# Optimization experiments

Measured on AMD Instinct MI355X. Metric: run time of the kernel, lower is better.

## Reference

```python
import jax, jax.numpy as jnp
import numpy as np

N_NODES = 50000
N_REL = 8
D_IN = 128
D_OUT = 128
N_EDGES = 800000


def setup_inputs() -> dict:
    key = jax.random.key(0)
    k = jax.random.split(key, 6)
    # Xavier-ish scales for the learned params
    w_scale = (6.0 / (D_IN + D_OUT)) ** 0.5
    X = jax.random.normal(k[0], (N_NODES, D_IN), dtype=jnp.float32)
    W = jax.random.uniform(k[1], (N_REL, D_IN, D_OUT), dtype=jnp.float32,
                           minval=-w_scale, maxval=w_scale)
    W0 = jax.random.uniform(k[2], (D_IN, D_OUT), dtype=jnp.float32,
                            minval=-w_scale, maxval=w_scale)
    inv_norm = jnp.ones((N_REL, N_NODES), dtype=jnp.float32)  # init'd to ones in torch
    # COO edge list encoding the stacked sparse adjacency tensor adj_tensor[r, dst, src]
    edge_src = jax.random.randint(k[3], (N_EDGES,), 0, N_NODES, dtype=jnp.int32)
    edge_dst = jax.random.randint(k[4], (N_EDGES,), 0, N_NODES, dtype=jnp.int32)
    edge_rel = jax.random.randint(k[5], (N_EDGES,), 0, N_REL, dtype=jnp.int32)
    return {"X": X, "W": W, "W0": W0, "inv_norm": inv_norm,
            "edge_src": edge_src, "edge_dst": edge_dst, "edge_rel": edge_rel}


def reference(X, W, W0, inv_norm, edge_src, edge_dst, edge_rel) -> jnp.ndarray:
    # Per relation r:  inv_norm[r][:,None] * (A_r @ (X @ W[r]))  ; summed over r
    R, N = inv_norm.shape
    # Dense per-relation transform: [R, N, D_OUT]
    XW = jnp.einsum('nd,rde->rne', X, W)
    # Sparse A_r @ XW_r as gather over source nodes + scatter-add into (rel, dst)
    msgs = XW[edge_rel, edge_src]                       # [E, D_OUT]
    seg_ids = edge_rel * N + edge_dst                   # combined (rel, dst) segment id
    agg = jax.ops.segment_sum(msgs, seg_ids, num_segments=R * N)
    agg = agg.reshape(R, N, -1)                         # [R, N, D_OUT]
    incoming = jnp.sum(agg * inv_norm[:, :, None], axis=0)  # [N, D_OUT]
    self_connection = X @ W0
    return incoming + self_connection
```

## Files before the change

kernel.cpp:

```cpp
#include <hip/hip_runtime.h>

typedef __attribute__((ext_vector_type(8))) short short8;
typedef __attribute__((ext_vector_type(4))) float f32x4;

__device__ __forceinline__ unsigned short f2bf(float f) {
    unsigned u = __float_as_uint(f);
    u += 0x7FFF + ((u >> 16) & 1);
    return (unsigned short)(u >> 16);
}

__device__ __forceinline__ float readlane_f(float v, int l) {
    return __int_as_float(__builtin_amdgcn_readlane(__float_as_int(v), l));
}

__device__ __forceinline__ float bflo(unsigned u) { return __uint_as_float(u << 16); }
__device__ __forceinline__ float bfhi(unsigned u) { return __uint_as_float(u & 0xFFFF0000u); }

#define CHB 2048
__global__ __launch_bounds__(256) void chist_kernel(
    const int* __restrict__ edst, int* __restrict__ ccounts, int E, int C)
{
    __shared__ int lh[CHB];
    const int t = threadIdx.x;
    for (int i = t; i < C; i += 256) lh[i] = 0;
    __syncthreads();
    const int base = blockIdx.x * 2048;
    const int end = min(base + 2048, E);
    for (int i = base + t; i < end; i += 256)
        atomicAdd(&lh[edst[i] >> 8], 1);
    __syncthreads();
    for (int i = t; i < C; i += 256)
        if (lh[i]) atomicAdd(&ccounts[i], lh[i]);
}

__global__ __launch_bounds__(256) void cscan_kernel(
    const int* __restrict__ ccounts, int* __restrict__ cstarts,
    int* __restrict__ cursor, int C)
{
    __shared__ int sd[256];
    const int t = threadIdx.x;
    const int per = (C + 255) >> 8;
    int c[8]; int s = 0;
#pragma unroll
    for (int k = 0; k < 8; ++k) {
        const int idx = t * per + k;
        c[k] = (k < per && idx < C) ? ccounts[idx] : 0;
        s += c[k];
    }
    sd[t] = s; __syncthreads();
    for (int off = 1; off < 256; off <<= 1) {
        int x = (t >= off) ? sd[t - off] : 0;
        __syncthreads();
        sd[t] += x;
        __syncthreads();
    }
    int run = sd[t] - s;
#pragma unroll
    for (int k = 0; k < 8; ++k) {
        const int idx = t * per + k;
        if (k < per && idx < C) { cstarts[idx] = run; cursor[idx] = run; }
        run += c[k];
    }
}

#define PART_EPB 2048
__global__ __launch_bounds__(256) void partition_kernel(
    const int* __restrict__ esrc, const int* __restrict__ edst,
    const int* __restrict__ erel, int* __restrict__ cursor,
    unsigned* __restrict__ staged, int E, int C)
{
    __shared__ int lh[CHB];
    const int t = threadIdx.x;
    const int base = blockIdx.x * PART_EPB;
    const int end = min(base + PART_EPB, E);

    for (int i = t; i < C; i += 256) lh[i] = 0;
    __syncthreads();
    for (int i = base + t; i < end; i += 256)
        atomicAdd(&lh[edst[i] >> 8], 1);
    __syncthreads();
    for (int i = t; i < C; i += 256) {
        const int c = lh[i];
        lh[i] = c ? atomicAdd(&cursor[i], c) : 0;
    }
    __syncthreads();
    for (int i = base + t; i < end; i += 256) {
        const int d = edst[i];
        const int pos = atomicAdd(&lh[d >> 8], 1);
        staged[pos] = (unsigned)esrc[i] | ((unsigned)(d & 255) << 21)
                    | ((unsigned)erel[i] << 29);
    }
}

__global__ __launch_bounds__(256) void binsort_kernel(
    const unsigned* __restrict__ staged, const int* __restrict__ cstarts,
    int* __restrict__ starts, unsigned* __restrict__ sorted,
    int N, int E, int C)
{
    __shared__ int lcur[2048];
    __shared__ int wsum[256];
    const int b = blockIdx.x;
    const int t = threadIdx.x;
    const int d0 = b << 8;
    const int binBase = d0 * 8;
    const int nbins = (min(d0 + 256, N) - d0) * 8;
    const int base = cstarts[b];
    const int end = (b + 1 < C) ? cstarts[b + 1] : E;

    for (int i = t; i < 2048; i += 256) lcur[i] = 0;
    __syncthreads();
    for (int i = base + t; i < end; i += 256) {
        const unsigned v = staged[i];
        atomicAdd(&lcur[(int)((v >> 21) & 255u) * 8 + (int)(v >> 29)], 1);
    }
    __syncthreads();
    const int b8 = t * 8;
    int c[8]; int s = 0;
#pragma unroll
    for (int k = 0; k < 8; ++k) { c[k] = lcur[b8 + k]; s += c[k]; }
    wsum[t] = s; __syncthreads();
    for (int off = 1; off < 256; off <<= 1) {
        int x = (t >= off) ? wsum[t - off] : 0;
        __syncthreads();
        wsum[t] += x;
        __syncthreads();
    }
    int run = wsum[t] - s + base;
#pragma unroll
    for (int k = 0; k < 8; ++k) {
        lcur[b8 + k] = run;
        if (b8 + k < nbins) starts[binBase + b8 + k] = run;
        run += c[k];
    }
    __syncthreads();
    for (int i = base + t; i < end; i += 256) {
        const unsigned v = staged[i];
        const unsigned src = v & 0x1FFFFFu;
        const unsigned rel = v >> 29;
        const int pos = atomicAdd(&lcur[(int)((v >> 21) & 255u) * 8 + (int)rel], 1);
        sorted[pos] = src | (rel << 28);
    }
}

__global__ __launch_bounds__(256) void cast_kernel(
    const float* __restrict__ X, const float* __restrict__ W,
    const float* __restrict__ W0, unsigned short* __restrict__ Xb,
    unsigned short* __restrict__ Bt, int M, int R)
{
    const int ktot = (R + 1) * 128;
    const int nx = M * 32;
    const int idx = blockIdx.x * 256 + threadIdx.x;
    if (idx < nx) {
        const float4 v = ((const float4*)X)[idx];
        uint2 p;
        p.x = (unsigned)f2bf(v.x) | ((unsigned)f2bf(v.y) << 16);
        p.y = (unsigned)f2bf(v.z) | ((unsigned)f2bf(v.w) << 16);
        *(uint2*)(Xb + (size_t)idx * 4) = p;
    } else if (idx < nx + 128 * ktot) {
        const int e = idx - nx;
        const int n = e / ktot;
        const int k = e - n * ktot;
        const float v = (k < R * 128) ? W[(size_t)k * 128 + n]
                                      : W0[(size_t)(k - R * 128) * 128 + n];
        Bt[(size_t)n * ktot + k] = f2bf(v);
    }
}

#define ACC(P, U) switch ((P) >> 28) {                                   \
        case 0: ax0 += bflo(U); ay0 += bfhi(U); break;                   \
        case 1: ax1 += bflo(U); ay1 += bfhi(U); break;                   \
        case 2: ax2 += bflo(U); ay2 += bfhi(U); break;                   \
        case 3: ax3 += bflo(U); ay3 += bfhi(U); break;                   \
        case 4: ax4 += bflo(U); ay4 += bfhi(U); break;                   \
        case 5: ax5 += bflo(U); ay5 += bfhi(U); break;                   \
        case 6: ax6 += bflo(U); ay6 += bfhi(U); break;                   \
        default: ax7 += bflo(U); ay7 += bfhi(U); break; }

__global__ __launch_bounds__(256) void aggregate_kernel(
    const unsigned short* __restrict__ Xb, const float* __restrict__ inv_norm,
    const unsigned* __restrict__ sorted, const int* __restrict__ starts,
    unsigned short* __restrict__ A, int N, int E)
{
    const int dst = (int)((blockIdx.x * blockDim.x + threadIdx.x) >> 6);
    if (dst >= N) return;
    const int lane = threadIdx.x & 63;

    const int start = starts[dst * 8];
    const int end = (dst + 1 < N) ? starts[dst * 8 + 8] : E;

    float ax0=0,ay0=0, ax1=0,ay1=0, ax2=0,ay2=0, ax3=0,ay3=0;
    float ax4=0,ay4=0, ax5=0,ay5=0, ax6=0,ay6=0, ax7=0,ay7=0;

    for (int cb = start; cb < end; cb += 64) {
        const int take = min(64, end - cb);
        unsigned batch = 0;
        if (cb + lane < end) batch = sorted[cb + lane];
        int j = 0;
        for (; j + 8 <= take; j += 8) {
            unsigned p[8], u[8];
#pragma unroll
            for (int q = 0; q < 8; ++q)
                p[q] = (unsigned)__builtin_amdgcn_readlane((int)batch, j + q);
#pragma unroll
            for (int q = 0; q < 8; ++q)
                u[q] = ((const unsigned*)(Xb + ((size_t)(p[q] & 0x0FFFFFFFu) << 7)))[lane];
            ACC(p[0], u[0]); ACC(p[1], u[1]); ACC(p[2], u[2]); ACC(p[3], u[3]);
            ACC(p[4], u[4]); ACC(p[5], u[5]); ACC(p[6], u[6]); ACC(p[7], u[7]);
        }
        for (; j + 4 <= take; j += 4) {
            const unsigned p0 = (unsigned)__builtin_amdgcn_readlane((int)batch, j);
            const unsigned p1 = (unsigned)__builtin_amdgcn_readlane((int)batch, j + 1);
            const unsigned p2 = (unsigned)__builtin_amdgcn_readlane((int)batch, j + 2);
            const unsigned p3 = (unsigned)__builtin_amdgcn_readlane((int)batch, j + 3);
            const unsigned u0 = ((const unsigned*)(Xb + ((size_t)(p0 & 0x0FFFFFFFu) << 7)))[lane];
            const unsigned u1 = ((const unsigned*)(Xb + ((size_t)(p1 & 0x0FFFFFFFu) << 7)))[lane];
            const unsigned u2 = ((const unsigned*)(Xb + ((size_t)(p2 & 0x0FFFFFFFu) << 7)))[lane];
            const unsigned u3 = ((const unsigned*)(Xb + ((size_t)(p3 & 0x0FFFFFFFu) << 7)))[lane];
            ACC(p0, u0); ACC(p1, u1); ACC(p2, u2); ACC(p3, u3);
        }
        for (; j < take; ++j) {
            const unsigned p = (unsigned)__builtin_amdgcn_readlane((int)batch, j);
            const unsigned u = ((const unsigned*)(Xb + ((size_t)(p & 0x0FFFFFFFu) << 7)))[lane];
            ACC(p, u);
        }
    }

    const float nv_l = (lane < 8) ? inv_norm[(size_t)lane * N + dst] : 0.f;

    unsigned short* Arow = A + (size_t)dst * 1024 + lane * 2;
    {
        float s;
        s = readlane_f(nv_l, 0); *(unsigned*)(Arow + 0*128) = (unsigned)f2bf(ax0*s) | ((unsigned)f2bf(ay0*s) << 16);
        s = readlane_f(nv_l, 1); *(unsigned*)(Arow + 1*128) = (unsigned)f2bf(ax1*s) | ((unsigned)f2bf(ay1*s) << 16);
        s = readlane_f(nv_l, 2); *(unsigned*)(Arow + 2*128) = (unsigned)f2bf(ax2*s) | ((unsigned)f2bf(ay2*s) << 16);
        s = readlane_f(nv_l, 3); *(unsigned*)(Arow + 3*128) = (unsigned)f2bf(ax3*s) | ((unsigned)f2bf(ay3*s) << 16);
        s = readlane_f(nv_l, 4); *(unsigned*)(Arow + 4*128) = (unsigned)f2bf(ax4*s) | ((unsigned)f2bf(ay4*s) << 16);
        s = readlane_f(nv_l, 5); *(unsigned*)(Arow + 5*128) = (unsigned)f2bf(ax5*s) | ((unsigned)f2bf(ay5*s) << 16);
        s = readlane_f(nv_l, 6); *(unsigned*)(Arow + 6*128) = (unsigned)f2bf(ax6*s) | ((unsigned)f2bf(ay6*s) << 16);
        s = readlane_f(nv_l, 7); *(unsigned*)(Arow + 7*128) = (unsigned)f2bf(ax7*s) | ((unsigned)f2bf(ay7*s) << 16);
    }
}

template <int KT>
__global__ __launch_bounds__(512) void gemm_kernel(
    const unsigned short* __restrict__ A, const unsigned short* __restrict__ Xb,
    const unsigned short* __restrict__ Bt, float* __restrict__ out, int M)
{
    constexpr int NI = KT / 64;
    constexpr int NA = (KT - 128) / 64;
    __shared__ unsigned short Asw[2][128 * 64];
    __shared__ unsigned short Bsw[2][128 * 64];

    const int tid = threadIdx.x;
    const int wave = tid >> 6;
    const int lane = tid & 63;
    const int ln = lane & 15, quad = lane >> 4;
    const int wm = wave & 3;
    const int wn = wave >> 2;
    const int m0 = blockIdx.x * 128;

    const int sr = tid >> 2;
    const int sq = tid & 3;
    int am = m0 + sr; if (am >= M) am = M - 1;
    const unsigned short* Ag = A  + (size_t)am * (KT - 128) + sq * 16;
    const unsigned short* Xg = Xb + (size_t)am * 128 + sq * 16;
    const unsigned short* Bg = Bt + (size_t)sr * KT + sq * 16;

    const int wofs0 = sr * 64 + ((((sq << 1) + 0) ^ (sr & 7)) << 3);
    const int wofs1 = sr * 64 + ((((sq << 1) + 1) ^ (sr & 7)) << 3);

    f32x4 acc[8] = {};
    short8 ra0, ra1, rb0, rb1;

    auto load_regs = [&](int ko) {
        const unsigned short* as = (ko < NA) ? (Ag + ko * 64) : (Xg + (ko - NA) * 64);
        ra0 = *(const short8*)(as);
        ra1 = *(const short8*)(as + 8);
        const unsigned short* bs = Bg + ko * 64;
        rb0 = *(const short8*)(bs);
        rb1 = *(const short8*)(bs + 8);
    };
    auto write_lds = [&](int buf) {
        *(short8*)&Asw[buf][wofs0] = ra0;
        *(short8*)&Asw[buf][wofs1] = ra1;
        *(short8*)&Bsw[buf][wofs0] = rb0;
        *(short8*)&Bsw[buf][wofs1] = rb1;
    };

    load_regs(0);
    write_lds(0);
    __syncthreads();

    int cur = 0;
#pragma unroll
    for (int ko = 0; ko < NI; ++ko) {
        if (ko + 1 < NI) load_regs(ko + 1);
        __builtin_amdgcn_sched_barrier(0);
#pragma unroll
        for (int ks = 0; ks < 2; ++ks) {
            short8 af[2], bf[4];
#pragma unroll
            for (int mi = 0; mi < 2; ++mi) {
                const int r = wm * 32 + mi * 16 + ln;
                af[mi] = *(const short8*)&Asw[cur][r * 64 + ((((ks << 2) + quad) ^ (r & 7)) << 3)];
            }
#pragma unroll
            for (int ci = 0; ci < 4; ++ci) {
                const int r = wn * 64 + ci * 16 + ln;
                bf[ci] = *(const short8*)&Bsw[cur][r * 64 + ((((ks << 2) + quad) ^ (r & 7)) << 3)];
            }
#pragma unroll
            for (int mi = 0; mi < 2; ++mi)
#pragma unroll
                for (int ci = 0; ci < 4; ++ci)
                    acc[mi * 4 + ci] = __builtin_amdgcn_mfma_f32_16x16x32_bf16(
                        af[mi], bf[ci], acc[mi * 4 + ci], 0, 0, 0);
        }
        __builtin_amdgcn_sched_barrier(0);
        if (ko + 1 < NI) write_lds(cur ^ 1);
        __syncthreads();
        cur ^= 1;
    }

#pragma unroll
    for (int mi = 0; mi < 2; ++mi)
#pragma unroll
        for (int ci = 0; ci < 4; ++ci)
#pragma unroll
            for (int rg = 0; rg < 4; ++rg) {
                const int row = m0 + wm * 32 + mi * 16 + quad * 4 + rg;
                if (row < M)
                    out[(size_t)row * 128 + wn * 64 + ci * 16 + ln] = acc[mi * 4 + ci][rg];
            }
}

__global__ __launch_bounds__(256) void gemm_kernel_rt(
    const unsigned short* __restrict__ A, const unsigned short* __restrict__ Xb,
    const unsigned short* __restrict__ Bt, float* __restrict__ out,
    int M, int ktot)
{
    const int tid = threadIdx.x;
    const int wave = tid >> 6;
    const int lane = tid & 63;
    const int ln = lane & 15, quad = lane >> 4;
    const int m0 = blockIdx.x * 64 + wave * 16;
    int m = m0 + ln; if (m >= M) m = M - 1;
    const unsigned short* Arow = A + (size_t)m * (ktot - 128) + quad * 8;
    const unsigned short* Xrow = Xb + (size_t)m * 128 + quad * 8;
    const unsigned short* Bbase = Bt + (size_t)ln * ktot + quad * 8;

    f32x4 acc[8] = {};
    for (int kb = 0; kb < (ktot >> 5); ++kb) {
        const int k0 = kb << 5;
        const unsigned short* asrc = (k0 < ktot - 128) ? (Arow + k0) : (Xrow + (k0 - (ktot - 128)));
        const short8 a = *(const short8*)asrc;
#pragma unroll
        for (int c = 0; c < 8; ++c) {
            const short8 b = *(const short8*)(Bbase + (size_t)c * 16 * ktot + k0);
            acc[c] = __builtin_amdgcn_mfma_f32_16x16x32_bf16(a, b, acc[c], 0, 0, 0);
        }
    }
#pragma unroll
    for (int c = 0; c < 8; ++c) {
#pragma unroll
        for (int rg = 0; rg < 4; ++rg) {
            const int row = m0 + quad * 4 + rg;
            if (row < M) out[(size_t)row * 128 + c * 16 + ln] = acc[c][rg];
        }
    }
}

extern "C" void kernel_launch(void* const* d_in, const int* in_sizes, int n_in,
                              void* d_out, int out_size, void* d_ws, size_t ws_size,
                              hipStream_t stream) {
    const float* X        = (const float*)d_in[0];
    const float* W        = (const float*)d_in[1];
    const float* W0       = (const float*)d_in[2];
    const float* inv_norm = (const float*)d_in[3];
    const int*   esrc     = (const int*)d_in[4];
    const int*   edst     = (const int*)d_in[5];
    const int*   erel     = (const int*)d_in[6];
    float* out = (float*)d_out;

    const int N  = in_sizes[0] / 128;
    const int E  = in_sizes[4];
    const int R  = in_sizes[3] / N;
    const int KB = N * 8;
    const int ktot = (R + 1) * 128;
    const int C  = (N + 255) >> 8;

    char* ws = (char*)d_ws;
    size_t off = 0;
    auto alloc = [&](size_t bytes) -> char* {
        char* p = ws + off; off = (off + bytes + 255) & ~(size_t)255; return p;
    };
    unsigned short* A         = (unsigned short*)alloc((size_t)N * R * 128 * 2);
    unsigned short* Xb        = (unsigned short*)alloc((size_t)N * 128 * 2);
    unsigned short* Bt        = (unsigned short*)alloc((size_t)128 * ktot * 2);
    int*            ccounts   = (int*)alloc((size_t)C * 4);
    int*            cstarts   = (int*)alloc((size_t)C * 4);
    int*            cursor    = (int*)alloc((size_t)C * 4);
    int*            starts    = (int*)alloc((size_t)KB * 4);
    unsigned*       staged    = (unsigned*)alloc((size_t)E * 4);
    unsigned*       sorted    = (unsigned*)alloc((size_t)E * 4);
    (void)ws_size;

    const int nEdgeBlocks = (E + 2047) / 2048;

    hipMemsetAsync(ccounts, 0, (size_t)C * 4, stream);
    chist_kernel<<<nEdgeBlocks, 256, 0, stream>>>(edst, ccounts, E, C);
    cscan_kernel<<<1, 256, 0, stream>>>(ccounts, cstarts, cursor, C);
    partition_kernel<<<nEdgeBlocks, 256, 0, stream>>>(esrc, edst, erel, cursor, staged, E, C);
    binsort_kernel<<<C, 256, 0, stream>>>(staged, cstarts, starts, sorted, N, E, C);
    cast_kernel<<<(N * 32 + 128 * ktot + 255) / 256, 256, 0, stream>>>(X, W, W0, Xb, Bt, N, R);
    aggregate_kernel<<<(N + 3) / 4, 256, 0, stream>>>(Xb, inv_norm, sorted, starts, A, N, E);
    if (ktot == 1152)
        gemm_kernel<1152><<<(N + 127) / 128, 512, 0, stream>>>(A, Xb, Bt, out, N);
    else
        gemm_kernel_rt<<<(N + 63) / 64, 256, 0, stream>>>(A, Xb, Bt, out, N, ktot);
}
```

Measured before the change: 207.3 us.

## Split GEMM output columns across two blocks and deepen aggregate gather unroll

The aggregation loop gains a 16-edge unrolled stage, so more independent row gathers are in flight before accumulation. The GEMM now tiles N into two 64-column halves, doubling the grid from about 391 to about 782 blocks for better CU coverage. Each block has half the B tile, which lowers LDS use and the accumulator count. In exchange, A tiles (the large K=1152 aggregated matrix) are read twice from global memory/L2, and the 16-deep unroll adds register pressure.

```diff
diff --git a/kernel.cpp b/kernel.cpp
--- a/kernel.cpp
+++ b/kernel.cpp
@@ -196,6 +196,17 @@
         unsigned batch = 0;
         if (cb + lane < end) batch = sorted[cb + lane];
         int j = 0;
+        for (; j + 16 <= take; j += 16) {
+            unsigned p[16], u[16];
+#pragma unroll
+            for (int q = 0; q < 16; ++q)
+                p[q] = (unsigned)__builtin_amdgcn_readlane((int)batch, j + q);
+#pragma unroll
+            for (int q = 0; q < 16; ++q)
+                u[q] = ((const unsigned*)(Xb + ((size_t)(p[q] & 0x0FFFFFFFu) << 7)))[lane];
+#pragma unroll
+            for (int q = 0; q < 16; ++q) { ACC(p[q], u[q]); }
+        }
         for (; j + 8 <= take; j += 8) {
             unsigned p[8], u[8];
 #pragma unroll
@@ -204,8 +215,8 @@
 #pragma unroll
             for (int q = 0; q < 8; ++q)
                 u[q] = ((const unsigned*)(Xb + ((size_t)(p[q] & 0x0FFFFFFFu) << 7)))[lane];
-            ACC(p[0], u[0]); ACC(p[1], u[1]); ACC(p[2], u[2]); ACC(p[3], u[3]);
-            ACC(p[4], u[4]); ACC(p[5], u[5]); ACC(p[6], u[6]); ACC(p[7], u[7]);
+#pragma unroll
+            for (int q = 0; q < 8; ++q) { ACC(p[q], u[q]); }
         }
         for (; j + 4 <= take; j += 4) {
             const unsigned p0 = (unsigned)__builtin_amdgcn_readlane((int)batch, j);
@@ -249,7 +260,7 @@
     constexpr int NI = KT / 64;
     constexpr int NA = (KT - 128) / 64;
     __shared__ unsigned short Asw[2][128 * 64];
-    __shared__ unsigned short Bsw[2][128 * 64];
+    __shared__ unsigned short Bsw[2][64 * 64];
 
     const int tid = threadIdx.x;
     const int wave = tid >> 6;
@@ -257,34 +268,36 @@
     const int ln = lane & 15, quad = lane >> 4;
     const int wm = wave & 3;
     const int wn = wave >> 2;
-    const int m0 = blockIdx.x * 128;
+    const int bm = blockIdx.x >> 1;
+    const int n0 = (blockIdx.x & 1) << 6;
+    const int m0 = bm * 128;
 
     const int sr = tid >> 2;
     const int sq = tid & 3;
     int am = m0 + sr; if (am >= M) am = M - 1;
     const unsigned short* Ag = A  + (size_t)am * (KT - 128) + sq * 16;
     const unsigned short* Xg = Xb + (size_t)am * 128 + sq * 16;
-    const unsigned short* Bg = Bt + (size_t)sr * KT + sq * 16;
-
-    const int wofs0 = sr * 64 + ((((sq << 1) + 0) ^ (sr & 7)) << 3);
-    const int wofs1 = sr * 64 + ((((sq << 1) + 1) ^ (sr & 7)) << 3);
-
-    f32x4 acc[8] = {};
-    short8 ra0, ra1, rb0, rb1;
+    const int br = tid >> 3;
+    const int bq = tid & 7;
+    const unsigned short* Bg = Bt + (size_t)(n0 + br) * KT + bq * 8;
+
+    const int wofsA0 = sr * 64 + ((((sq << 1) + 0) ^ (sr & 7)) << 3);
+    const int wofsA1 = sr * 64 + ((((sq << 1) + 1) ^ (sr & 7)) << 3);
+    const int wofsB  = br * 64 + ((bq ^ (br & 7)) << 3);
+
+    f32x4 acc[4] = {};
+    short8 ra0, ra1, rb0;
 
     auto load_regs = [&](int ko) {
         const unsigned short* as = (ko < NA) ? (Ag + ko * 64) : (Xg + (ko - NA) * 64);
         ra0 = *(const short8*)(as);
         ra1 = *(const short8*)(as + 8);
-        const unsigned short* bs = Bg + ko * 64;
-        rb0 = *(const short8*)(bs);
-        rb1 = *(const short8*)(bs + 8);
+        rb0 = *(const short8*)(Bg + ko * 64);
     };
     auto write_lds = [&](int buf) {
-        *(short8*)&Asw[buf][wofs0] = ra0;
-        *(short8*)&Asw[buf][wofs1] = ra1;
-        *(short8*)&Bsw[buf][wofs0] = rb0;
-        *(short8*)&Bsw[buf][wofs1] = rb1;
+        *(short8*)&Asw[buf][wofsA0] = ra0;
+        *(short8*)&Asw[buf][wofsA1] = ra1;
+        *(short8*)&Bsw[buf][wofsB]  = rb0;
     };
 
     load_regs(0);
@@ -298,23 +311,23 @@
         __builtin_amdgcn_sched_barrier(0);
 #pragma unroll
         for (int ks = 0; ks < 2; ++ks) {
-            short8 af[2], bf[4];
+            short8 af[2], bf[2];
 #pragma unroll
             for (int mi = 0; mi < 2; ++mi) {
                 const int r = wm * 32 + mi * 16 + ln;
                 af[mi] = *(const short8*)&Asw[cur][r * 64 + ((((ks << 2) + quad) ^ (r & 7)) << 3)];
             }
 #pragma unroll
-            for (int ci = 0; ci < 4; ++ci) {
-                const int r = wn * 64 + ci * 16 + ln;
+            for (int ci = 0; ci < 2; ++ci) {
+                const int r = wn * 32 + ci * 16 + ln;
                 bf[ci] = *(const short8*)&Bsw[cur][r * 64 + ((((ks << 2) + quad) ^ (r & 7)) << 3)];
             }
 #pragma unroll
             for (int mi = 0; mi < 2; ++mi)
 #pragma unroll
-                for (int ci = 0; ci < 4; ++ci)
-                    acc[mi * 4 + ci] = __builtin_amdgcn_mfma_f32_16x16x32_bf16(
-                        af[mi], bf[ci], acc[mi * 4 + ci], 0, 0, 0);
+                for (int ci = 0; ci < 2; ++ci)
+                    acc[mi * 2 + ci] = __builtin_amdgcn_mfma_f32_16x16x32_bf16(
+                        af[mi], bf[ci], acc[mi * 2 + ci], 0, 0, 0);
         }
         __builtin_amdgcn_sched_barrier(0);
         if (ko + 1 < NI) write_lds(cur ^ 1);
@@ -325,12 +338,12 @@
 #pragma unroll
     for (int mi = 0; mi < 2; ++mi)
 #pragma unroll
-        for (int ci = 0; ci < 4; ++ci)
+        for (int ci = 0; ci < 2; ++ci)
 #pragma unroll
             for (int rg = 0; rg < 4; ++rg) {
                 const int row = m0 + wm * 32 + mi * 16 + quad * 4 + rg;
                 if (row < M)
-                    out[(size_t)row * 128 + wn * 64 + ci * 16 + ln] = acc[mi * 4 + ci][rg];
+                    out[(size_t)row * 128 + n0 + wn * 32 + ci * 16 + ln] = acc[mi * 2 + ci][rg];
             }
 }
 
@@ -415,7 +428,7 @@
     cast_kernel<<<(N * 32 + 128 * ktot + 255) / 256, 256, 0, stream>>>(X, W, W0, Xb, Bt, N, R);
     aggregate_kernel<<<(N + 3) / 4, 256, 0, stream>>>(Xb, inv_norm, sorted, starts, A, N, E);
     if (ktot == 1152)
-        gemm_kernel<1152><<<(N + 127) / 128, 512, 0, stream>>>(A, Xb, Bt, out, N);
+        gemm_kernel<1152><<<((N + 127) / 128) * 2, 512, 0, stream>>>(A, Xb, Bt, out, N);
     else
         gemm_kernel_rt<<<(N + 63) / 64, 256, 0, stream>>>(A, Xb, Bt, out, N, ktot);
 }
```

After: 221.2 us. 6.7% more time.

## Reorder to transform-then-aggregate: precompute X·W per relation, then gather-sum messages

Applied to the files above, without the earlier changes.

Computes Y = X·[W_r | W0] for all relations with an MFMA GEMM first, writing relation slices as bf16 and the self-connection directly to the output. A new aggregation kernel then gathers per-edge rows from Y, scales them by inv_norm and adds them into the output. This removes the large intermediate aggregated matrix and the K=1152 GEMM over it. In exchange, the edge gathers read from a table nine times larger than X, which reduces cache locality. The old unrolled aggregate loops are simplified and kept only for the fallback path.

```diff
diff --git a/kernel.cpp b/kernel.cpp
--- a/kernel.cpp
+++ b/kernel.cpp
@@ -166,6 +166,123 @@
     }
 }
 
+template <int KT>
+__global__ __launch_bounds__(256) void ygemm_kernel(
+    const unsigned short* __restrict__ Xb, const unsigned short* __restrict__ Bt,
+    unsigned short* __restrict__ Y, float* __restrict__ out, int M)
+{
+    __shared__ unsigned short Xsw[64 * 128];
+    __shared__ unsigned short Bsw[128 * 128];
+    const int tid = threadIdx.x;
+    const int wave = tid >> 6, lane = tid & 63;
+    const int ln = lane & 15, quad = lane >> 4;
+    const int m0 = blockIdx.x * 64;
+    const int w = blockIdx.y;
+    const int kofs = w << 7;
+
+    {
+        const int r = tid >> 2, q = tid & 3;
+        int am = m0 + r; if (am >= M) am = M - 1;
+        const unsigned short* src = Xb + (size_t)am * 128 + q * 32;
+#pragma unroll
+        for (int i = 0; i < 4; ++i) {
+            const int c = q * 4 + i;
+            *(short8*)&Xsw[r * 128 + (((c ^ (r & 7)) & 15) << 3)] = *(const short8*)(src + i * 8);
+        }
+    }
+    {
+        const int r = tid >> 1, q = tid & 1;
+        const unsigned short* src = Bt + (size_t)r * KT + kofs + q * 64;
+#pragma unroll
+        for (int i = 0; i < 8; ++i) {
+            const int c = q * 8 + i;
+            *(short8*)&Bsw[r * 128 + (((c ^ (r & 7)) & 15) << 3)] = *(const short8*)(src + i * 8);
+        }
+    }
+    __syncthreads();
+
+    f32x4 acc[8] = {};
+#pragma unroll
+    for (int ks = 0; ks < 4; ++ks) {
+        const int ar = wave * 16 + ln;
+        const short8 a = *(const short8*)&Xsw[ar * 128 + ((((ks * 4 + quad) ^ (ar & 7)) & 15) << 3)];
+#pragma unroll
+        for (int c = 0; c < 8; ++c) {
+            const int br = c * 16 + ln;
+            const short8 b = *(const short8*)&Bsw[br * 128 + ((((ks * 4 + quad) ^ (br & 7)) & 15) << 3)];
+            acc[c] = __builtin_amdgcn_mfma_f32_16x16x32_bf16(a, b, acc[c], 0, 0, 0);
+        }
+    }
+
+    if (w < 8) {
+#pragma unroll
+        for (int c = 0; c < 8; ++c)
+#pragma unroll
+            for (int rg = 0; rg < 4; ++rg) {
+                const int row = m0 + wave * 16 + quad * 4 + rg;
+                if (row < M)
+                    Y[(size_t)row * 1152 + kofs + c * 16 + ln] = f2bf(acc[c][rg]);
+            }
+    } else {
+#pragma unroll
+        for (int c = 0; c < 8; ++c)
+#pragma unroll
+            for (int rg = 0; rg < 4; ++rg) {
+                const int row = m0 + wave * 16 + quad * 4 + rg;
+                if (row < M)
+                    out[(size_t)row * 128 + c * 16 + ln] = acc[c][rg];
+            }
+    }
+}
+
+__global__ __launch_bounds__(256) void aggregate2_kernel(
+    const unsigned short* __restrict__ Y, const float* __restrict__ inv_norm,
+    const unsigned* __restrict__ sorted, const int* __restrict__ starts,
+    float* __restrict__ out, int N, int E)
+{
+    const int dst = (int)((blockIdx.x * blockDim.x + threadIdx.x) >> 6);
+    if (dst >= N) return;
+    const int lane = threadIdx.x & 63;
+
+    const int start = starts[dst * 8];
+    const int end = (dst + 1 < N) ? starts[dst * 8 + 8] : E;
+
+    const float nv_l = (lane < 8) ? inv_norm[(size_t)lane * N + dst] : 0.f;
+
+    float ox = 0.f, oy = 0.f;
+    for (int cb = start; cb < end; cb += 64) {
+        const int take = min(64, end - cb);
+        unsigned batch = 0;
+        if (cb + lane < end) batch = sorted[cb + lane];
+        int j = 0;
+        for (; j + 8 <= take; j += 8) {
+            unsigned p[8], u[8]; float s[8];
+#pragma unroll
+            for (int q = 0; q < 8; ++q)
+                p[q] = (unsigned)__builtin_amdgcn_readlane((int)batch, j + q);
+#pragma unroll
+            for (int q = 0; q < 8; ++q)
+                u[q] = ((const unsigned*)(Y + (size_t)(p[q] & 0x0FFFFFFFu) * 1152
+                                            + ((p[q] >> 28) << 7)))[lane];
+#pragma unroll
+            for (int q = 0; q < 8; ++q) s[q] = readlane_f(nv_l, (int)(p[q] >> 28));
+#pragma unroll
+            for (int q = 0; q < 8; ++q) { ox += s[q] * bflo(u[q]); oy += s[q] * bfhi(u[q]); }
+        }
+        for (; j < take; ++j) {
+            const unsigned p = (unsigned)__builtin_amdgcn_readlane((int)batch, j);
+            const unsigned u = ((const unsigned*)(Y + (size_t)(p & 0x0FFFFFFFu) * 1152
+                                                    + ((p >> 28) << 7)))[lane];
+            const float s = readlane_f(nv_l, (int)(p >> 28));
+            ox += s * bflo(u); oy += s * bfhi(u);
+        }
+    }
+
+    float2 o = *(float2*)&out[(size_t)dst * 128 + lane * 2];
+    o.x += ox; o.y += oy;
+    *(float2*)&out[(size_t)dst * 128 + lane * 2] = o;
+}
+
 #define ACC(P, U) switch ((P) >> 28) {                                   \
         case 0: ax0 += bflo(U); ay0 += bfhi(U); break;                   \
         case 1: ax1 += bflo(U); ay1 += bfhi(U); break;                   \
@@ -195,30 +312,7 @@
         const int take = min(64, end - cb);
         unsigned batch = 0;
         if (cb + lane < end) batch = sorted[cb + lane];
-        int j = 0;
-        for (; j + 8 <= take; j += 8) {
-            unsigned p[8], u[8];
-#pragma unroll
-            for (int q = 0; q < 8; ++q)
-                p[q] = (unsigned)__builtin_amdgcn_readlane((int)batch, j + q);
-#pragma unroll
-            for (int q = 0; q < 8; ++q)
-                u[q] = ((const unsigned*)(Xb + ((size_t)(p[q] & 0x0FFFFFFFu) << 7)))[lane];
-            ACC(p[0], u[0]); ACC(p[1], u[1]); ACC(p[2], u[2]); ACC(p[3], u[3]);
-            ACC(p[4], u[4]); ACC(p[5], u[5]); ACC(p[6], u[6]); ACC(p[7], u[7]);
-        }
-        for (; j + 4 <= take; j += 4) {
-            const unsigned p0 = (unsigned)__builtin_amdgcn_readlane((int)batch, j);
-            const unsigned p1 = (unsigned)__builtin_amdgcn_readlane((int)batch, j + 1);
-            const unsigned p2 = (unsigned)__builtin_amdgcn_readlane((int)batch, j + 2);
-            const unsigned p3 = (unsigned)__builtin_amdgcn_readlane((int)batch, j + 3);
-            const unsigned u0 = ((const unsigned*)(Xb + ((size_t)(p0 & 0x0FFFFFFFu) << 7)))[lane];
-            const unsigned u1 = ((const unsigned*)(Xb + ((size_t)(p1 & 0x0FFFFFFFu) << 7)))[lane];
-            const unsigned u2 = ((const unsigned*)(Xb + ((size_t)(p2 & 0x0FFFFFFFu) << 7)))[lane];
-            const unsigned u3 = ((const unsigned*)(Xb + ((size_t)(p3 & 0x0FFFFFFFu) << 7)))[lane];
-            ACC(p0, u0); ACC(p1, u1); ACC(p2, u2); ACC(p3, u3);
-        }
-        for (; j < take; ++j) {
+        for (int j = 0; j < take; ++j) {
             const unsigned p = (unsigned)__builtin_amdgcn_readlane((int)batch, j);
             const unsigned u = ((const unsigned*)(Xb + ((size_t)(p & 0x0FFFFFFFu) << 7)))[lane];
             ACC(p, u);
@@ -226,7 +320,6 @@
     }
 
     const float nv_l = (lane < 8) ? inv_norm[(size_t)lane * N + dst] : 0.f;
-
     unsigned short* Arow = A + (size_t)dst * 1024 + lane * 2;
     {
         float s;
@@ -241,99 +334,6 @@
     }
 }
 
-template <int KT>
-__global__ __launch_bounds__(512) void gemm_kernel(
-    const unsigned short* __restrict__ A, const unsigned short* __restrict__ Xb,
-    const unsigned short* __restrict__ Bt, float* __restrict__ out, int M)
-{
-    constexpr int NI = KT / 64;
-    constexpr int NA = (KT - 128) / 64;
-    __shared__ unsigned short Asw[2][128 * 64];
-    __shared__ unsigned short Bsw[2][128 * 64];
-
-    const int tid = threadIdx.x;
-    const int wave = tid >> 6;
-    const int lane = tid & 63;
-    const int ln = lane & 15, quad = lane >> 4;
-    const int wm = wave & 3;
-    const int wn = wave >> 2;
-    const int m0 = blockIdx.x * 128;
-
-    const int sr = tid >> 2;
-    const int sq = tid & 3;
-    int am = m0 + sr; if (am >= M) am = M - 1;
-    const unsigned short* Ag = A  + (size_t)am * (KT - 128) + sq * 16;
-    const unsigned short* Xg = Xb + (size_t)am * 128 + sq * 16;
-    const unsigned short* Bg = Bt + (size_t)sr * KT + sq * 16;
-
-    const int wofs0 = sr * 64 + ((((sq << 1) + 0) ^ (sr & 7)) << 3);
-    const int wofs1 = sr * 64 + ((((sq << 1) + 1) ^ (sr & 7)) << 3);
-
-    f32x4 acc[8] = {};
-    short8 ra0, ra1, rb0, rb1;
-
-    auto load_regs = [&](int ko) {
-        const unsigned short* as = (ko < NA) ? (Ag + ko * 64) : (Xg + (ko - NA) * 64);
-        ra0 = *(const short8*)(as);
-        ra1 = *(const short8*)(as + 8);
-        const unsigned short* bs = Bg + ko * 64;
-        rb0 = *(const short8*)(bs);
-        rb1 = *(const short8*)(bs + 8);
-    };
-    auto write_lds = [&](int buf) {
-        *(short8*)&Asw[buf][wofs0] = ra0;
-        *(short8*)&Asw[buf][wofs1] = ra1;
-        *(short8*)&Bsw[buf][wofs0] = rb0;
-        *(short8*)&Bsw[buf][wofs1] = rb1;
-    };
-
-    load_regs(0);
-    write_lds(0);
-    __syncthreads();
-
-    int cur = 0;
-#pragma unroll
-    for (int ko = 0; ko < NI; ++ko) {
-        if (ko + 1 < NI) load_regs(ko + 1);
-        __builtin_amdgcn_sched_barrier(0);
-#pragma unroll
-        for (int ks = 0; ks < 2; ++ks) {
-            short8 af[2], bf[4];
-#pragma unroll
-            for (int mi = 0; mi < 2; ++mi) {
-                const int r = wm * 32 + mi * 16 + ln;
-                af[mi] = *(const short8*)&Asw[cur][r * 64 + ((((ks << 2) + quad) ^ (r & 7)) << 3)];
-            }
-#pragma unroll
-            for (int ci = 0; ci < 4; ++ci) {
-                const int r = wn * 64 + ci * 16 + ln;
-                bf[ci] = *(const short8*)&Bsw[cur][r * 64 + ((((ks << 2) + quad) ^ (r & 7)) << 3)];
-            }
-#pragma unroll
-            for (int mi = 0; mi < 2; ++mi)
-#pragma unroll
-                for (int ci = 0; ci < 4; ++ci)
-                    acc[mi * 4 + ci] = __builtin_amdgcn_mfma_f32_16x16x32_bf16(
-                        af[mi], bf[ci], acc[mi * 4 + ci], 0, 0, 0);
-        }
-        __builtin_amdgcn_sched_barrier(0);
-        if (ko + 1 < NI) write_lds(cur ^ 1);
-        __syncthreads();
-        cur ^= 1;
-    }
-
-#pragma unroll
-    for (int mi = 0; mi < 2; ++mi)
-#pragma unroll
-        for (int ci = 0; ci < 4; ++ci)
-#pragma unroll
-            for (int rg = 0; rg < 4; ++rg) {
-                const int row = m0 + wm * 32 + mi * 16 + quad * 4 + rg;
-                if (row < M)
-                    out[(size_t)row * 128 + wn * 64 + ci * 16 + ln] = acc[mi * 4 + ci][rg];
-            }
-}
-
 __global__ __launch_bounds__(256) void gemm_kernel_rt(
     const unsigned short* __restrict__ A, const unsigned short* __restrict__ Xb,
     const unsigned short* __restrict__ Bt, float* __restrict__ out,
@@ -394,7 +394,7 @@
     auto alloc = [&](size_t bytes) -> char* {
         char* p = ws + off; off = (off + bytes + 255) & ~(size_t)255; return p;
     };
-    unsigned short* A         = (unsigned short*)alloc((size_t)N * R * 128 * 2);
+    unsigned short* Y         = (unsigned short*)alloc((size_t)N * 1152 * 2);
     unsigned short* Xb        = (unsigned short*)alloc((size_t)N * 128 * 2);
     unsigned short* Bt        = (unsigned short*)alloc((size_t)128 * ktot * 2);
     int*            ccounts   = (int*)alloc((size_t)C * 4);
@@ -413,9 +413,13 @@
     partition_kernel<<<nEdgeBlocks, 256, 0, stream>>>(esrc, edst, erel, cursor, staged, E, C);
     binsort_kernel<<<C, 256, 0, stream>>>(staged, cstarts, starts, sorted, N, E, C);
     cast_kernel<<<(N * 32 + 128 * ktot + 255) / 256, 256, 0, stream>>>(X, W, W0, Xb, Bt, N, R);
-    aggregate_kernel<<<(N + 3) / 4, 256, 0, stream>>>(Xb, inv_norm, sorted, starts, A, N, E);
-    if (ktot == 1152)
-        gemm_kernel<1152><<<(N + 127) / 128, 512, 0, stream>>>(A, Xb, Bt, out, N);
-    else
+    if (ktot == 1152) {
+        dim3 yg((N + 63) / 64, 9);
+        ygemm_kernel<1152><<<yg, 256, 0, stream>>>(Xb, Bt, Y, out, N);
+        aggregate2_kernel<<<(N + 3) / 4, 256, 0, stream>>>(Y, inv_norm, sorted, starts, out, N, E);
+    } else {
+        unsigned short* A = Y;
+        aggregate_kernel<<<(N + 3) / 4, 256, 0, stream>>>(Xb, inv_norm, sorted, starts, A, N, E);
         gemm_kernel_rt<<<(N + 63) / 64, 256, 0, stream>>>(A, Xb, Bt, out, N, ktot);
-}
+    }
+}
```

Result: slower. 232.3 us (+12.1%).
